# Optimization experiments

Measured on AMD Instinct MI355X. Metric: run time of the kernel, lower is better.

Reference implementation:

```python
import jax, jax.numpy as jnp
import numpy as np

ANNEALING_SCALE = 0.1
BS, NV, S, D, V = 2, 16, 1024, 768, 50257

def setup_inputs() -> dict:
    key = jax.random.key(0)
    k1, k2, k3, k4, k5 = jax.random.split(key, 5)
    return {
        "input_ids": jax.random.randint(k1, (BS, S), 0, V),
        "content": jax.random.normal(k2, (BS, NV, S, D), dtype=jnp.float32),
        "contextualization": jax.random.normal(k3, (BS, NV, S, S), dtype=jnp.float32) * 0.05,
        "lm_head_weight": jax.random.normal(k4, (V, D), dtype=jnp.float32) * 0.02,
        "content_weights": jax.random.uniform(k5, (V, NV), dtype=jnp.float32),
    }

def reference(input_ids, content, contextualization, lm_head_weight, content_weights):
    bs, nv, s, d = content.shape
    # --- mask_annealing ---
    # Original computes relu(content @ W.T) over full vocab then gathers at input_ids.
    # Equivalent: gather rows of W first, then contract (same math since relu is
    # elementwise and only gathered columns are summed).
    Wg = lm_head_weight[input_ids]                              # (bs, s, d)
    sims = jnp.einsum('bkid,bjd->bkij', content, Wg)            # (bs, 16, s, s)
    sims = jnp.sum(jax.nn.relu(sims), axis=3)                   # (bs, 16, s)
    scores = jax.nn.sigmoid(-ANNEALING_SCALE * sims + 6.0)
    # upweight_nearby modifier
    scores = scores * (1.0 + jnp.arange(s, dtype=content.dtype) / 100.0)[None, None, :]
    scores = jnp.transpose(scores, (0, 2, 1))                   # (bs, s, 16)
    # --- create_content_soft_mask ---
    cw = content_weights[input_ids]                             # (bs, s, 16)
    weights = cw * scores + (1.0 - scores)                      # (bs, s, 16)
    # --- weighted sense combination ---
    content_m = content * jnp.transpose(weights, (0, 2, 1))[..., None]  # (bs,16,s,d)
    hidden = jnp.einsum('bkij,bkjd->bid', contextualization, content_m) # (bs, s, d)
    logits = hidden @ lm_head_weight.T                          # (bs, s, vocab)
    return logits
```

## Files before the change

### kernel.cpp

```cpp
#include <hip/hip_runtime.h>
#include <cstdint>
#include <cstddef>

#define BSZ 2
#define NV 16
#define SEQ 1024
#define DIM 768
#define VOC 50257
#define VOCP 50304

typedef unsigned int u32;
typedef unsigned short u16;
typedef _Float16 half8 __attribute__((ext_vector_type(8)));
typedef float f32x4 __attribute__((ext_vector_type(4)));

__device__ __forceinline__ u16 f2h(float f) {
  return __builtin_bit_cast(unsigned short, (_Float16)f);
}
__device__ __forceinline__ u32 pk2h(float a, float b) {
  return (u32)f2h(a) | ((u32)f2h(b) << 16);
}

__device__ __forceinline__ void gload16(const u16* g, u16* l) {
  __builtin_amdgcn_global_load_lds(
      (const __attribute__((address_space(1))) void*)g,
      (__attribute__((address_space(3))) void*)l, 16, 0, 0);
}

__global__ void k_prep_content(const float* __restrict__ content,
                               u16* __restrict__ cbf, u16* __restrict__ cT) {
  __shared__ u16 tile[64][70];
  const int bk = blockIdx.z;
  const int d0 = blockIdx.x * 64, j0 = blockIdx.y * 64;
  const float* src = content + (size_t)bk * SEQ * DIM;
  u16* dst = cbf + (size_t)bk * SEQ * DIM;
  u16* dstT = cT + (size_t)bk * DIM * SEQ;
  const int c4 = (threadIdx.x & 15) * 4;
  const int r0 = threadIdx.x >> 4;
#pragma unroll
  for (int it = 0; it < 4; ++it) {
    const int r = it * 16 + r0;
    const float4 f = *(const float4*)(src + (size_t)(j0 + r) * DIM + d0 + c4);
    const u32 lo = pk2h(f.x, f.y), hi = pk2h(f.z, f.w);
    *(uint2*)(dst + (size_t)(j0 + r) * DIM + d0 + c4) = make_uint2(lo, hi);
    *(u32*)&tile[r][c4] = lo;
    *(u32*)&tile[r][c4 + 2] = hi;
  }
  __syncthreads();
#pragma unroll
  for (int it = 0; it < 4; ++it) {
    const int dd = it * 16 + r0;
    const int j4 = c4;
    const u32 lo = (u32)tile[j4][dd] | ((u32)tile[j4 + 1][dd] << 16);
    const u32 hi = (u32)tile[j4 + 2][dd] | ((u32)tile[j4 + 3][dd] << 16);
    *(uint2*)(dstT + (size_t)(d0 + dd) * SEQ + j0 + j4) = make_uint2(lo, hi);
  }
}

__global__ void k_prep_w(const float* __restrict__ W, u16* __restrict__ Wb) {
  const int v = blockIdx.x;
  const int c = threadIdx.x * 4;
  u32 lo, hi;
  if (v < VOC) {
    const float4 f = *(const float4*)(W + (size_t)v * DIM + c);
    lo = pk2h(f.x, f.y); hi = pk2h(f.z, f.w);
  } else {
    lo = 0u; hi = 0u;
  }
  *(uint2*)(Wb + (size_t)v * DIM + c) = make_uint2(lo, hi);
}

__global__ void k_gather(const int* __restrict__ ids, const u16* __restrict__ Wb,
                         u16* __restrict__ Wg) {
  const int b = blockIdx.y, j = blockIdx.x;
  const int row = ids[b * SEQ + j];
  const int c = threadIdx.x * 4;
  *(uint2*)(Wg + ((size_t)b * SEQ + j) * DIM + c) =
      *(const uint2*)(Wb + (size_t)row * DIM + c);
}

__global__ void k_zero(float* __restrict__ p, int n) {
  const int i = blockIdx.x * 256 + threadIdx.x;
  if (i < n) p[i] = 0.f;
}

template <int LDA, int LDB>
__device__ __forceinline__ void gemm_ring1(const u16* __restrict__ A,
                                           const u16* __restrict__ B,
                                           u16* As, u16* Bs,
                                           f32x4 (&acc)[4][4], int t) {
  const int lane = t & 63, w = t >> 6, wr = w >> 1, wc = w & 1;
  const int rl = lane & 15;
  const int gsw = (((lane >> 4) ^ ((rl >> 1) & 3)) * 8);
  const int srow = 16 * w + (lane >> 2);
  const int sg = (((lane & 3) ^ ((lane >> 3) & 3)) * 8);
  const size_t gaBase = (size_t)srow * LDA + sg;
  const size_t gbBase = (size_t)srow * LDB + sg;
  const int wof = w * 512;

#define STG1_(ss, kt)                                                   \
  {                                                                     \
    const u16* ga_ = A + gaBase + (size_t)(kt) * 32;                    \
    const u16* gb_ = B + gbBase + (size_t)(kt) * 32;                    \
    gload16(ga_, As + (ss) * 4096 + wof);                               \
    gload16(ga_ + (size_t)64 * LDA, As + (ss) * 4096 + wof + 2048);     \
    gload16(gb_, Bs + (ss) * 4096 + wof);                               \
    gload16(gb_ + (size_t)64 * LDB, Bs + (ss) * 4096 + wof + 2048);     \
  }

  STG1_(0, 0);
  STG1_(1, 1);
#pragma unroll 1
  for (int kt = 0; kt < 32; ++kt) {
    if (kt < 31)
      asm volatile("s_waitcnt vmcnt(4)" ::: "memory");
    else
      asm volatile("s_waitcnt vmcnt(0)" ::: "memory");
    __builtin_amdgcn_s_barrier();
    __builtin_amdgcn_sched_barrier(0);
    const int ss = kt % 3;
    if (kt < 30) STG1_((kt + 2) % 3, kt + 2);
    half8 af[4], bf[4];
#pragma unroll
    for (int m = 0; m < 4; ++m)
      af[m] = *(const half8*)(As + ss * 4096 + (wr * 64 + m * 16 + rl) * 32 + gsw);
#pragma unroll
    for (int n = 0; n < 4; ++n)
      bf[n] = *(const half8*)(Bs + ss * 4096 + (wc * 64 + n * 16 + rl) * 32 + gsw);
    __builtin_amdgcn_s_setprio(1);
#pragma unroll
    for (int m = 0; m < 4; ++m)
#pragma unroll
      for (int n = 0; n < 4; ++n)
        acc[m][n] = __builtin_amdgcn_mfma_f32_16x16x32_f16(af[m], bf[n], acc[m][n], 0, 0, 0);
    __builtin_amdgcn_s_setprio(0);
  }
#undef STG1_
}

template <int LDA, int LDB>
__device__ __forceinline__ void gemm_ring2(const u16* __restrict__ A0,
                                           const u16* __restrict__ A1,
                                           const u16* __restrict__ B, int ksteps,
                                           u16* As0, u16* As1, u16* Bs,
                                           f32x4 (&acc0)[4][4],
                                           f32x4 (&acc1)[4][4], int t) {
  const int lane = t & 63, w = t >> 6, wr = w >> 1, wc = w & 1;
  const int rl = lane & 15;
  const int gsw = (((lane >> 4) ^ ((rl >> 1) & 3)) * 8);
  const int srow = 16 * w + (lane >> 2);
  const int sg = (((lane & 3) ^ ((lane >> 3) & 3)) * 8);
  const size_t gaBase = (size_t)srow * LDA + sg;
  const size_t gbBase = (size_t)srow * LDB + sg;
  const int wof = w * 512;

#define STG3_(ss, kt)                                                   \
  {                                                                     \
    const u16* ga0_ = A0 + gaBase + (size_t)(kt) * 32;                  \
    const u16* ga1_ = A1 + gaBase + (size_t)(kt) * 32;                  \
    const u16* gb_ = B + gbBase + (size_t)(kt) * 32;                    \
    gload16(ga0_, As0 + (ss) * 4096 + wof);                             \
    gload16(ga0_ + (size_t)64 * LDA, As0 + (ss) * 4096 + wof + 2048);   \
    gload16(ga1_, As1 + (ss) * 4096 + wof);                            \
    gload16(ga1_ + (size_t)64 * LDA, As1 + (ss) * 4096 + wof + 2048);   \
    gload16(gb_, Bs + (ss) * 4096 + wof);                              \
    gload16(gb_ + (size_t)64 * LDB, Bs + (ss) * 4096 + wof + 2048);     \
  }

#define FRAGS3_(ss)                                                     \
  half8 af0[4], af1[4], bf[4];                                          \
  _Pragma("unroll") for (int n = 0; n < 4; ++n)                         \
      bf[n] = *(const half8*)(Bs + (ss) * 4096 +                        \
                              (wc * 64 + n * 16 + rl) * 32 + gsw);      \
  _Pragma("unroll") for (int m = 0; m < 4; ++m)                         \
      af0[m] = *(const half8*)(As0 + (ss) * 4096 +                      \
                               (wr * 64 + m * 16 + rl) * 32 + gsw);     \
  _Pragma("unroll") for (int m = 0; m < 4; ++m)                         \
      af1[m] = *(const half8*)(As1 + (ss) * 4096 +                      \
                               (wr * 64 + m * 16 + rl) * 32 + gsw);

#define MFMA32_                                                         \
  __builtin_amdgcn_s_setprio(1);                                        \
  _Pragma("unroll") for (int m = 0; m < 4; ++m)                         \
      _Pragma("unroll") for (int n = 0; n < 4; ++n)                     \
          acc0[m][n] = __builtin_amdgcn_mfma_f32_16x16x32_f16(          \
              af0[m], bf[n], acc0[m][n], 0, 0, 0);                      \
  _Pragma("unroll") for (int m = 0; m < 4; ++m)                         \
      _Pragma("unroll") for (int n = 0; n < 4; ++n)                     \
          acc1[m][n] = __builtin_amdgcn_mfma_f32_16x16x32_f16(          \
              af1[m], bf[n], acc1[m][n], 0, 0, 0);                      \
  __builtin_amdgcn_s_setprio(0);

#define STEPF_(ss, kt)                                                  \
  asm volatile("s_waitcnt vmcnt(6)" ::: "memory");                      \
  __builtin_amdgcn_s_barrier();                                         \
  __builtin_amdgcn_sched_barrier(0);                                    \
  STG3_(((ss) + 2) % 3, (kt) + 2);                                      \
  { FRAGS3_(ss) MFMA32_ }

#define STEPL6_(ss)                                                     \
  asm volatile("s_waitcnt vmcnt(6)" ::: "memory");                      \
  __builtin_amdgcn_s_barrier();                                         \
  __builtin_amdgcn_sched_barrier(0);                                    \
  { FRAGS3_(ss) MFMA32_ }

#define STEPL0_(ss)                                                     \
  asm volatile("s_waitcnt vmcnt(0)" ::: "memory");                      \
  __builtin_amdgcn_s_barrier();                                         \
  __builtin_amdgcn_sched_barrier(0);                                    \
  { FRAGS3_(ss) MFMA32_ }

  STG3_(0, 0);
  STG3_(1, 1);
  const int nTrip = ksteps / 3;
  for (int u = 0; u < nTrip - 1; ++u) {
    const int kt = 3 * u;
    STEPF_(0, kt);
    STEPF_(1, kt + 1);
    STEPF_(2, kt + 2);
  }
  STEPF_(0, ksteps - 3);
  STEPL6_(1);
  STEPL0_(2);
#undef STG3_
#undef FRAGS3_
#undef MFMA32_
#undef STEPF_
#undef STEPL6_
#undef STEPL0_
}

__global__ __launch_bounds__(256, 2) void k_sims(const u16* __restrict__ cbf,
                                                 const u16* __restrict__ Wg,
                                                 float* __restrict__ sims) {
  __shared__ __align__(16) u16 As0[3 * 4096];
  __shared__ __align__(16) u16 As1[3 * 4096];
  __shared__ __align__(16) u16 Bs[3 * 4096];
  const int bk = blockIdx.z, b = bk >> 4;
  const int t = threadIdx.x;
  const int i0 = blockIdx.y * 256;
  const u16* A0 = cbf + (size_t)bk * SEQ * DIM + (size_t)i0 * DIM;
  const u16* A1 = A0 + (size_t)128 * DIM;
  const u16* B = Wg + (size_t)b * SEQ * DIM + (size_t)(blockIdx.x * 128) * DIM;
  f32x4 acc0[4][4] = {}, acc1[4][4] = {};
  gemm_ring2<DIM, DIM>(A0, A1, B, DIM / 32, As0, As1, Bs, acc0, acc1, t);
  const int lane = t & 63, w = t >> 6, wr = w >> 1;
  const int rg = lane >> 4, cl = lane & 15;
#pragma unroll
  for (int m = 0; m < 4; ++m) {
#pragma unroll
    for (int r = 0; r < 4; ++r) {
      float s0 = 0.f, s1 = 0.f;
#pragma unroll
      for (int n = 0; n < 4; ++n) {
        s0 += fmaxf(acc0[m][n][r], 0.f);
        s1 += fmaxf(acc1[m][n][r], 0.f);
      }
      s0 += __shfl_xor(s0, 1); s1 += __shfl_xor(s1, 1);
      s0 += __shfl_xor(s0, 2); s1 += __shfl_xor(s1, 2);
      s0 += __shfl_xor(s0, 4); s1 += __shfl_xor(s1, 4);
      s0 += __shfl_xor(s0, 8); s1 += __shfl_xor(s1, 8);
      if (cl == 0) {
        const int i = i0 + wr * 64 + m * 16 + rg * 4 + r;
        atomicAdd(&sims[(size_t)bk * SEQ + i], s0);
        atomicAdd(&sims[(size_t)bk * SEQ + i + 128], s1);
      }
    }
  }
}

__global__ void k_weights(const float* __restrict__ sims, const int* __restrict__ ids,
                          const float* __restrict__ cw, float* __restrict__ wtsT) {
  const int j = blockIdx.x * 256 + threadIdx.x;
  const int bk = blockIdx.y;
  const int b = bk >> 4, k = bk & 15;
  const float sm = sims[(size_t)bk * SEQ + j];
  float score = 1.f / (1.f + __expf(0.1f * sm - 6.f));
  score *= 1.f + (float)j * 0.01f;
  const int id = ids[b * SEQ + j];
  const float c = cw[(size_t)id * NV + k];
  wtsT[(size_t)bk * SEQ + j] = c * score + (1.f - score);
}

__global__ void k_ctx(const float* __restrict__ ctx, const float* __restrict__ wtsT,
                      u16* __restrict__ ctxw) {
  const size_t i = ((size_t)blockIdx.x * 256 + threadIdx.x) * 4;
  const float4 c = *(const float4*)(ctx + i);
  const size_t bk = i >> 20;
  const int j = (int)(i & (SEQ - 1));
  const float4 wv = *(const float4*)(wtsT + bk * SEQ + j);
  *(uint2*)(ctxw + i) =
      make_uint2(pk2h(c.x * wv.x, c.y * wv.y), pk2h(c.z * wv.z, c.w * wv.w));
}

__global__ __launch_bounds__(256, 3) void k_hidden(const u16* __restrict__ ctxw,
                                                   const u16* __restrict__ cT,
                                                   float* __restrict__ part) {
  __shared__ __align__(16) u16 As[3 * 4096];
  __shared__ __align__(16) u16 Bs[3 * 4096];
  const int z = blockIdx.z;
  const int b = z >> 3, g = z & 7;
  const int i0 = blockIdx.y * 128, d0 = blockIdx.x * 128;
  const int t = threadIdx.x;
  f32x4 acc[4][4] = {};
  for (int kk = 0; kk < 2; ++kk) {
    const int sense = g * 2 + kk;
    const u16* A = ctxw + ((size_t)(b * NV + sense) * SEQ + i0) * SEQ;
    const u16* B = cT + ((size_t)(b * NV + sense) * DIM + d0) * SEQ;
    gemm_ring1<SEQ, SEQ>(A, B, As, Bs, acc, t);
    __syncthreads();
  }
  const int lane = t & 63, w = t >> 6, wr = w >> 1, wc = w & 1;
  const int rg = lane >> 4, cl = lane & 15;
  float* P = part + ((size_t)(g * BSZ + b) * SEQ + i0) * DIM + d0;
#pragma unroll
  for (int m = 0; m < 4; ++m)
#pragma unroll
    for (int n = 0; n < 4; ++n)
#pragma unroll
      for (int r = 0; r < 4; ++r)
        P[(size_t)(wr * 64 + m * 16 + rg * 4 + r) * DIM + wc * 64 + n * 16 + cl] =
            acc[m][n][r];
}

__global__ void k_reduce(const float* __restrict__ part, u16* __restrict__ hid) {
  const size_t i = ((size_t)blockIdx.x * 256 + threadIdx.x) * 4;
  const size_t NHID = (size_t)BSZ * SEQ * DIM;
  float4 s = {0.f, 0.f, 0.f, 0.f};
#pragma unroll
  for (int g = 0; g < 8; ++g) {
    const float4 p = *(const float4*)(part + (size_t)g * NHID + i);
    s.x += p.x; s.y += p.y; s.z += p.z; s.w += p.w;
  }
  *(uint2*)(hid + i) = make_uint2(pk2h(s.x, s.y), pk2h(s.z, s.w));
}

__global__ __launch_bounds__(256, 2) void k_logits(const u16* __restrict__ hid,
                                                   const u16* __restrict__ Wb,
                                                   float* __restrict__ out) {
  __shared__ __align__(16) u16 lds[3 * 12288];
  const int bid = blockIdx.x;
  const int swz = (bid & 7) * 393 + (bid >> 3);
  const int it = swz & 7, vt = swz >> 3;
  const int i0 = it * 256, v0 = vt * 128;
  const int t = threadIdx.x;
  const int lane = t & 63, w = t >> 6;
  const int wm = w >> 1, wn = w & 1;
  const int rl = lane & 15, kg = lane >> 4;
  const int gsw = (kg ^ ((rl >> 1) & 3)) * 8;
  const int srow = t >> 2;
  const int sgr = ((t & 3) ^ ((srow >> 1) & 3)) * 8;
  const u16* Abase = hid + ((size_t)i0 + srow) * DIM + sgr;
  const u16* Bbase = Wb + ((size_t)v0 + srow) * DIM + sgr;
  u16* dls = lds + t * 8;

#define STG(ss, koff)                                                 \
  {                                                                   \
    const u16* a_ = Abase + (koff);                                   \
    u16* d_ = dls + (ss) * 12288;                                     \
    gload16(a_, d_);                                                  \
    gload16(a_ + (size_t)64 * DIM, d_ + 2048);                        \
    gload16(a_ + (size_t)128 * DIM, d_ + 4096);                       \
    gload16(a_ + (size_t)192 * DIM, d_ + 6144);                       \
    const u16* b_ = Bbase + (koff);                                   \
    gload16(b_, d_ + 8192);                                           \
    gload16(b_ + (size_t)64 * DIM, d_ + 10240);                       \
  }

#define CMP(ss)                                                       \
  {                                                                   \
    half8 af[8], bf[4];                                               \
    _Pragma("unroll") for (int n = 0; n < 4; ++n)                     \
        bf[n] = *(const half8*)(lds + (ss) * 12288 + 8192 +           \
                                (wn * 64 + n * 16 + rl) * 32 + gsw);  \
    _Pragma("unroll") for (int m = 0; m < 8; ++m)                     \
        af[m] = *(const half8*)(lds + (ss) * 12288 +                  \
                                (wm * 128 + m * 16 + rl) * 32 + gsw); \
    __builtin_amdgcn_s_setprio(1);                                    \
    _Pragma("unroll") for (int m = 0; m < 8; ++m)                     \
        _Pragma("unroll") for (int n = 0; n < 4; ++n)                 \
            acc[m][n] = __builtin_amdgcn_mfma_f32_16x16x32_f16(       \
                af[m], bf[n], acc[m][n], 0, 0, 0);                    \
    __builtin_amdgcn_s_setprio(0);                                    \
  }

#define BARS                                                          \
  __builtin_amdgcn_s_barrier();                                       \
  __builtin_amdgcn_sched_barrier(0);

#define STEPF(ss, st, koff)                                           \
  asm volatile("s_waitcnt vmcnt(6)" ::: "memory");                    \
  BARS;                                                               \
  STG(st, koff);                                                      \
  CMP(ss)

  f32x4 acc[8][4] = {};
  STG(0, 0);
  STG(1, 32);
#pragma unroll 1
  for (int u = 0; u < 7; ++u) {
    const int kb = u * 96;
    STEPF(0, 2, kb + 64);
    STEPF(1, 0, kb + 96);
    STEPF(2, 1, kb + 128);
  }
  STEPF(0, 2, 736);
  asm volatile("s_waitcnt vmcnt(6)" ::: "memory");
  BARS;
  CMP(1);
  asm volatile("s_waitcnt vmcnt(0)" ::: "memory");
  BARS;
  CMP(2);
#undef STG
#undef CMP
#undef BARS
#undef STEPF

#pragma unroll
  for (int m = 0; m < 8; ++m)
#pragma unroll
    for (int n = 0; n < 4; ++n) {
      const int vv = v0 + wn * 64 + n * 16 + rl;
      if (vv < VOC) {
        const int ib = i0 + wm * 128 + m * 16 + kg * 4;
#pragma unroll
        for (int r = 0; r < 4; ++r)
          out[(size_t)(ib + r) * VOC + vv] = acc[m][n][r];
      }
    }
}

extern "C" void kernel_launch(void* const* d_in, const int* in_sizes, int n_in,
                              void* d_out, int out_size, void* d_ws, size_t ws_size,
                              hipStream_t stream) {
  const int* ids = (const int*)d_in[0];
  const float* content = (const float*)d_in[1];
  const float* ctx = (const float*)d_in[2];
  const float* W = (const float*)d_in[3];
  const float* cw = (const float*)d_in[4];
  float* out = (float*)d_out;
  char* ws = (char*)d_ws;

  u16* cbf  = (u16*)(ws);
  u16* cT   = (u16*)(ws + 50331648);
  u16* Wb   = (u16*)(ws + 100663296);
  u16* Wg   = (u16*)(ws + 177930240);
  u16* ctxw = (u16*)(ws + 181075968);
  float* sims = (float*)(ws + 248184832);
  float* wtsT = (float*)(ws + 248315904);
  float* part = (float*)cbf;
  u16* hid = Wg;

  k_prep_content<<<dim3(DIM / 64, SEQ / 64, BSZ * NV), 256, 0, stream>>>(
      content, cbf, cT);
  k_prep_w<<<VOCP, 192, 0, stream>>>(W, Wb);
  k_gather<<<dim3(SEQ, BSZ), 192, 0, stream>>>(ids, Wb, Wg);
  k_zero<<<128, 256, 0, stream>>>(sims, BSZ * NV * SEQ);
  k_sims<<<dim3(8, 4, BSZ * NV), 256, 0, stream>>>(cbf, Wg, sims);
  k_weights<<<dim3(4, BSZ * NV), 256, 0, stream>>>(sims, ids, cw, wtsT);
  k_ctx<<<32768, 256, 0, stream>>>(ctx, wtsT, ctxw);
  k_hidden<<<dim3(6, 8, 16), 256, 0, stream>>>(ctxw, cT, part);
  k_reduce<<<1536, 256, 0, stream>>>(part, hid);
  k_logits<<<8 * 393, 256, 0, stream>>>(hid, Wb, out);
}
```

Measured before the change: 564.1 us.

## Give each wave private LDS tiles to drop block barriers in logits GEMM

The logits GEMM now has each wave stage its own 128x32 A slice and 64x32 B slice into a private region of LDS with a 3-deep ring. Block-wide s_barrier calls are gone and waves sync only through vmcnt/lgkmcnt waits. This removes barrier stalls between waves but duplicates A/B loads across waves, raises LDS use to 144KB, and drops occupancy to one block per CU. Separately, the weight fp16 conversion kernel becomes a grid-stride flat loop with 2048 blocks instead of one block per vocabulary row.

```diff
diff --git a/kernel.cpp b/kernel.cpp
--- a/kernel.cpp
+++ b/kernel.cpp
@@ -58,16 +58,17 @@
 }
 
 __global__ void k_prep_w(const float* __restrict__ W, u16* __restrict__ Wb) {
-  const int v = blockIdx.x;
-  const int c = threadIdx.x * 4;
-  u32 lo, hi;
-  if (v < VOC) {
-    const float4 f = *(const float4*)(W + (size_t)v * DIM + c);
-    lo = pk2h(f.x, f.y); hi = pk2h(f.z, f.w);
-  } else {
-    lo = 0u; hi = 0u;
-  }
-  *(uint2*)(Wb + (size_t)v * DIM + c) = make_uint2(lo, hi);
+  const size_t nW = (size_t)VOC * DIM / 4;
+  const size_t total = (size_t)VOCP * DIM / 4;
+  for (size_t u = (size_t)blockIdx.x * 256 + threadIdx.x; u < total;
+       u += (size_t)gridDim.x * 256) {
+    u32 lo = 0u, hi = 0u;
+    if (u < nW) {
+      const float4 f = *(const float4*)(W + u * 4);
+      lo = pk2h(f.x, f.y); hi = pk2h(f.z, f.w);
+    }
+    *(uint2*)(Wb + u * 4) = make_uint2(lo, hi);
+  }
 }
 
 __global__ void k_gather(const int* __restrict__ ids, const u16* __restrict__ Wb,
@@ -335,10 +336,10 @@
   *(uint2*)(hid + i) = make_uint2(pk2h(s.x, s.y), pk2h(s.z, s.w));
 }
 
-__global__ __launch_bounds__(256, 2) void k_logits(const u16* __restrict__ hid,
+__global__ __launch_bounds__(256, 1) void k_logits(const u16* __restrict__ hid,
                                                    const u16* __restrict__ Wb,
                                                    float* __restrict__ out) {
-  __shared__ __align__(16) u16 lds[3 * 12288];
+  __shared__ __align__(16) u16 lds[4 * 3 * 6144];
   const int bid = blockIdx.x;
   const int swz = (bid & 7) * 393 + (bid >> 3);
   const int it = swz & 7, vt = swz >> 3;
@@ -348,73 +349,64 @@
   const int wm = w >> 1, wn = w & 1;
   const int rl = lane & 15, kg = lane >> 4;
   const int gsw = (kg ^ ((rl >> 1) & 3)) * 8;
-  const int srow = t >> 2;
-  const int sgr = ((t & 3) ^ ((srow >> 1) & 3)) * 8;
-  const u16* Abase = hid + ((size_t)i0 + srow) * DIM + sgr;
-  const u16* Bbase = Wb + ((size_t)v0 + srow) * DIM + sgr;
-  u16* dls = lds + t * 8;
-
-#define STG(ss, koff)                                                 \
-  {                                                                   \
-    const u16* a_ = Abase + (koff);                                   \
-    u16* d_ = dls + (ss) * 12288;                                     \
-    gload16(a_, d_);                                                  \
-    gload16(a_ + (size_t)64 * DIM, d_ + 2048);                        \
-    gload16(a_ + (size_t)128 * DIM, d_ + 4096);                       \
-    gload16(a_ + (size_t)192 * DIM, d_ + 6144);                       \
-    const u16* b_ = Bbase + (koff);                                   \
-    gload16(b_, d_ + 8192);                                           \
-    gload16(b_ + (size_t)64 * DIM, d_ + 10240);                       \
-  }
-
-#define CMP(ss)                                                       \
-  {                                                                   \
-    half8 af[8], bf[4];                                               \
-    _Pragma("unroll") for (int n = 0; n < 4; ++n)                     \
-        bf[n] = *(const half8*)(lds + (ss) * 12288 + 8192 +           \
-                                (wn * 64 + n * 16 + rl) * 32 + gsw);  \
-    _Pragma("unroll") for (int m = 0; m < 8; ++m)                     \
-        af[m] = *(const half8*)(lds + (ss) * 12288 +                  \
-                                (wm * 128 + m * 16 + rl) * 32 + gsw); \
-    __builtin_amdgcn_s_setprio(1);                                    \
-    _Pragma("unroll") for (int m = 0; m < 8; ++m)                     \
-        _Pragma("unroll") for (int n = 0; n < 4; ++n)                 \
-            acc[m][n] = __builtin_amdgcn_mfma_f32_16x16x32_f16(       \
-                af[m], bf[n], acc[m][n], 0, 0, 0);                    \
-    __builtin_amdgcn_s_setprio(0);                                    \
-  }
-
-#define BARS                                                          \
-  __builtin_amdgcn_s_barrier();                                       \
-  __builtin_amdgcn_sched_barrier(0);
-
-#define STEPF(ss, st, koff)                                           \
-  asm volatile("s_waitcnt vmcnt(6)" ::: "memory");                    \
-  BARS;                                                               \
-  STG(st, koff);                                                      \
-  CMP(ss)
+  const int sgr = ((lane & 3) ^ ((lane >> 3) & 3)) * 8;
+  const u16* Aw = hid + ((size_t)i0 + wm * 128 + (lane >> 2)) * DIM + sgr;
+  const u16* Bw = Wb + ((size_t)v0 + wn * 64 + (lane >> 2)) * DIM + sgr;
+  u16* wbase = lds + w * 18432;
+  u16* dls = wbase + lane * 8;
+
+#define STG(ss, koff)                                                  \
+  {                                                                    \
+    const u16* a_ = Aw + (koff);                                       \
+    u16* d_ = dls + (ss) * 6144;                                       \
+    gload16(a_, d_);                                                   \
+    gload16(a_ + (size_t)16 * DIM, d_ + 512);                          \
+    gload16(a_ + (size_t)32 * DIM, d_ + 1024);                         \
+    gload16(a_ + (size_t)48 * DIM, d_ + 1536);                         \
+    gload16(a_ + (size_t)64 * DIM, d_ + 2048);                         \
+    gload16(a_ + (size_t)80 * DIM, d_ + 2560);                         \
+    gload16(a_ + (size_t)96 * DIM, d_ + 3072);                         \
+    gload16(a_ + (size_t)112 * DIM, d_ + 3584);                        \
+    const u16* b_ = Bw + (koff);                                       \
+    u16* e_ = d_ + 4096;                                               \
+    gload16(b_, e_);                                                   \
+    gload16(b_ + (size_t)16 * DIM, e_ + 512);                          \
+    gload16(b_ + (size_t)32 * DIM, e_ + 1024);                         \
+    gload16(b_ + (size_t)48 * DIM, e_ + 1536);                         \
+  }
 
   f32x4 acc[8][4] = {};
   STG(0, 0);
   STG(1, 32);
 #pragma unroll 1
-  for (int u = 0; u < 7; ++u) {
-    const int kb = u * 96;
-    STEPF(0, 2, kb + 64);
-    STEPF(1, 0, kb + 96);
-    STEPF(2, 1, kb + 128);
-  }
-  STEPF(0, 2, 736);
-  asm volatile("s_waitcnt vmcnt(6)" ::: "memory");
-  BARS;
-  CMP(1);
-  asm volatile("s_waitcnt vmcnt(0)" ::: "memory");
-  BARS;
-  CMP(2);
+  for (int k = 0; k < 24; ++k) {
+    if (k < 23)
+      asm volatile("s_waitcnt vmcnt(12)" ::: "memory");
+    else
+      asm volatile("s_waitcnt vmcnt(0)" ::: "memory");
+    __builtin_amdgcn_sched_barrier(0);
+    const int ss = k % 3;
+    const u16* sa = wbase + ss * 6144;
+    half8 af[8], bf[4];
+#pragma unroll
+    for (int n = 0; n < 4; ++n)
+      bf[n] = *(const half8*)(sa + 4096 + (n * 16 + rl) * 32 + gsw);
+#pragma unroll
+    for (int m = 0; m < 8; ++m)
+      af[m] = *(const half8*)(sa + (m * 16 + rl) * 32 + gsw);
+    if (k < 22) STG((k + 2) % 3, (k + 2) * 32);
+    asm volatile("s_waitcnt lgkmcnt(0)" ::: "memory");
+    __builtin_amdgcn_sched_barrier(0);
+    __builtin_amdgcn_s_setprio(1);
+#pragma unroll
+    for (int m = 0; m < 8; ++m)
+#pragma unroll
+      for (int n = 0; n < 4; ++n)
+        acc[m][n] =
+            __builtin_amdgcn_mfma_f32_16x16x32_f16(af[m], bf[n], acc[m][n], 0, 0, 0);
+    __builtin_amdgcn_s_setprio(0);
+  }
 #undef STG
-#undef CMP
-#undef BARS
-#undef STEPF
 
 #pragma unroll
   for (int m = 0; m < 8; ++m)
@@ -453,7 +445,7 @@
 
   k_prep_content<<<dim3(DIM / 64, SEQ / 64, BSZ * NV), 256, 0, stream>>>(
       content, cbf, cT);
-  k_prep_w<<<VOCP, 192, 0, stream>>>(W, Wb);
+  k_prep_w<<<2048, 256, 0, stream>>>(W, Wb);
   k_gather<<<dim3(SEQ, BSZ), 192, 0, stream>>>(ids, Wb, Wg);
   k_zero<<<128, 256, 0, stream>>>(sims, BSZ * NV * SEQ);
   k_sims<<<dim3(8, 4, BSZ * NV), 256, 0, stream>>>(cbf, Wg, sims);
```

Result: slower. 651.0 us (+15.4%).

## Fuse context weighting into hidden GEMM with register-staged loads

Applied to the files above, without the earlier changes.

Removes the separate k_ctx pass that wrote a weighted fp16 copy of the 128MB contextualization tensor. k_hidden now reads the fp32 context and sense weights directly, multiplies and converts them in registers, then stores the result to a double-buffered LDS tile. This replaces the async global-to-LDS triple-buffer ring with a register prefetch and two barriers per k-step. Blocks are remapped to a 1D grid so that co-resident blocks share content tiles. k_prep_w also becomes a grid-stride kernel. The fused loop reads fp32 (twice the bytes of fp16) and has less prefetch depth, which could leave the MFMA units waiting on memory.

```diff
diff --git a/kernel.cpp b/kernel.cpp
--- a/kernel.cpp
+++ b/kernel.cpp
@@ -58,16 +58,17 @@
 }
 
 __global__ void k_prep_w(const float* __restrict__ W, u16* __restrict__ Wb) {
-  const int v = blockIdx.x;
-  const int c = threadIdx.x * 4;
-  u32 lo, hi;
-  if (v < VOC) {
-    const float4 f = *(const float4*)(W + (size_t)v * DIM + c);
-    lo = pk2h(f.x, f.y); hi = pk2h(f.z, f.w);
-  } else {
-    lo = 0u; hi = 0u;
-  }
-  *(uint2*)(Wb + (size_t)v * DIM + c) = make_uint2(lo, hi);
+  const size_t nW = (size_t)VOC * DIM / 4;
+  const size_t total = (size_t)VOCP * DIM / 4;
+  for (size_t u = (size_t)blockIdx.x * 256 + threadIdx.x; u < total;
+       u += (size_t)gridDim.x * 256) {
+    u32 lo = 0u, hi = 0u;
+    if (u < nW) {
+      const float4 f = *(const float4*)(W + u * 4);
+      lo = pk2h(f.x, f.y); hi = pk2h(f.z, f.w);
+    }
+    *(uint2*)(Wb + u * 4) = make_uint2(lo, hi);
+  }
 }
 
 __global__ void k_gather(const int* __restrict__ ids, const u16* __restrict__ Wb,
@@ -82,60 +83,6 @@
 __global__ void k_zero(float* __restrict__ p, int n) {
   const int i = blockIdx.x * 256 + threadIdx.x;
   if (i < n) p[i] = 0.f;
-}
-
-template <int LDA, int LDB>
-__device__ __forceinline__ void gemm_ring1(const u16* __restrict__ A,
-                                           const u16* __restrict__ B,
-                                           u16* As, u16* Bs,
-                                           f32x4 (&acc)[4][4], int t) {
-  const int lane = t & 63, w = t >> 6, wr = w >> 1, wc = w & 1;
-  const int rl = lane & 15;
-  const int gsw = (((lane >> 4) ^ ((rl >> 1) & 3)) * 8);
-  const int srow = 16 * w + (lane >> 2);
-  const int sg = (((lane & 3) ^ ((lane >> 3) & 3)) * 8);
-  const size_t gaBase = (size_t)srow * LDA + sg;
-  const size_t gbBase = (size_t)srow * LDB + sg;
-  const int wof = w * 512;
-
-#define STG1_(ss, kt)                                                   \
-  {                                                                     \
-    const u16* ga_ = A + gaBase + (size_t)(kt) * 32;                    \
-    const u16* gb_ = B + gbBase + (size_t)(kt) * 32;                    \
-    gload16(ga_, As + (ss) * 4096 + wof);                               \
-    gload16(ga_ + (size_t)64 * LDA, As + (ss) * 4096 + wof + 2048);     \
-    gload16(gb_, Bs + (ss) * 4096 + wof);                               \
-    gload16(gb_ + (size_t)64 * LDB, Bs + (ss) * 4096 + wof + 2048);     \
-  }
-
-  STG1_(0, 0);
-  STG1_(1, 1);
-#pragma unroll 1
-  for (int kt = 0; kt < 32; ++kt) {
-    if (kt < 31)
-      asm volatile("s_waitcnt vmcnt(4)" ::: "memory");
-    else
-      asm volatile("s_waitcnt vmcnt(0)" ::: "memory");
-    __builtin_amdgcn_s_barrier();
-    __builtin_amdgcn_sched_barrier(0);
-    const int ss = kt % 3;
-    if (kt < 30) STG1_((kt + 2) % 3, kt + 2);
-    half8 af[4], bf[4];
-#pragma unroll
-    for (int m = 0; m < 4; ++m)
-      af[m] = *(const half8*)(As + ss * 4096 + (wr * 64 + m * 16 + rl) * 32 + gsw);
-#pragma unroll
-    for (int n = 0; n < 4; ++n)
-      bf[n] = *(const half8*)(Bs + ss * 4096 + (wc * 64 + n * 16 + rl) * 32 + gsw);
-    __builtin_amdgcn_s_setprio(1);
-#pragma unroll
-    for (int m = 0; m < 4; ++m)
-#pragma unroll
-      for (int n = 0; n < 4; ++n)
-        acc[m][n] = __builtin_amdgcn_mfma_f32_16x16x32_f16(af[m], bf[n], acc[m][n], 0, 0, 0);
-    __builtin_amdgcn_s_setprio(0);
-  }
-#undef STG1_
 }
 
 template <int LDA, int LDB>
@@ -282,37 +229,95 @@
   wtsT[(size_t)bk * SEQ + j] = c * score + (1.f - score);
 }
 
-__global__ void k_ctx(const float* __restrict__ ctx, const float* __restrict__ wtsT,
-                      u16* __restrict__ ctxw) {
-  const size_t i = ((size_t)blockIdx.x * 256 + threadIdx.x) * 4;
-  const float4 c = *(const float4*)(ctx + i);
-  const size_t bk = i >> 20;
-  const int j = (int)(i & (SEQ - 1));
-  const float4 wv = *(const float4*)(wtsT + bk * SEQ + j);
-  *(uint2*)(ctxw + i) =
-      make_uint2(pk2h(c.x * wv.x, c.y * wv.y), pk2h(c.z * wv.z, c.w * wv.w));
-}
-
-__global__ __launch_bounds__(256, 3) void k_hidden(const u16* __restrict__ ctxw,
+__global__ __launch_bounds__(256, 3) void k_hidden(const float* __restrict__ ctx,
+                                                   const float* __restrict__ wtsT,
                                                    const u16* __restrict__ cT,
                                                    float* __restrict__ part) {
-  __shared__ __align__(16) u16 As[3 * 4096];
-  __shared__ __align__(16) u16 Bs[3 * 4096];
-  const int z = blockIdx.z;
-  const int b = z >> 3, g = z & 7;
-  const int i0 = blockIdx.y * 128, d0 = blockIdx.x * 128;
+  __shared__ __align__(16) u16 As[2 * 4096];
+  __shared__ __align__(16) u16 Bs[2 * 4096];
+  const int L = blockIdx.x;
+  const int g8 = L & 7, q = L >> 3;
+  const int p = g8 * 16 + q / 6;
+  const int dt = q % 6;
+  const int y = p & 7, z = p >> 3;
+  const int b = z >> 3, grp = z & 7;
+  const int i0 = y * 128, d0 = dt * 128;
   const int t = threadIdx.x;
+  const int lane = t & 63, w = t >> 6, wr = w >> 1, wc = w & 1;
+  const int rl = lane & 15;
+  const int gsw = (((lane >> 4) ^ ((rl >> 1) & 3)) * 8);
+  const int srow = 16 * w + (lane >> 2);
+  const int sg = (((lane & 3) ^ ((lane >> 3) & 3)) * 8);
+
   f32x4 acc[4][4] = {};
-  for (int kk = 0; kk < 2; ++kk) {
-    const int sense = g * 2 + kk;
-    const u16* A = ctxw + ((size_t)(b * NV + sense) * SEQ + i0) * SEQ;
-    const u16* B = cT + ((size_t)(b * NV + sense) * DIM + d0) * SEQ;
-    gemm_ring1<SEQ, SEQ>(A, B, As, Bs, acc, t);
+  float4 ra0, ra1, ra2, ra3, rw0, rw1;
+  uint4 rb0, rb1;
+
+#define LDREGS(u_)                                                      \
+  {                                                                     \
+    const int s_ = (u_) >> 5, kt_ = (u_) & 31;                          \
+    const size_t bkq_ = (size_t)b * NV + grp * 2 + s_;                  \
+    const int jsw_ = kt_ * 32 + sg;                                     \
+    const float* ap_ = ctx + (bkq_ * SEQ + i0 + srow) * SEQ + jsw_;     \
+    ra0 = *(const float4*)(ap_);                                        \
+    ra1 = *(const float4*)(ap_ + 4);                                    \
+    ra2 = *(const float4*)(ap_ + (size_t)64 * SEQ);                     \
+    ra3 = *(const float4*)(ap_ + (size_t)64 * SEQ + 4);                 \
+    const float* wp_ = wtsT + bkq_ * SEQ + jsw_;                        \
+    rw0 = *(const float4*)(wp_);                                        \
+    rw1 = *(const float4*)(wp_ + 4);                                    \
+    const u16* bp_ = cT + (bkq_ * DIM + d0 + srow) * SEQ + jsw_;        \
+    rb0 = *(const uint4*)(bp_);                                         \
+    rb1 = *(const uint4*)(bp_ + (size_t)64 * SEQ);                      \
+  }
+
+#define WRITE(cc)                                                       \
+  {                                                                     \
+    u16* da_ = As + (cc) * 4096 + w * 512 + lane * 8;                   \
+    *(uint4*)(da_) =                                                    \
+        make_uint4(pk2h(ra0.x * rw0.x, ra0.y * rw0.y),                  \
+                   pk2h(ra0.z * rw0.z, ra0.w * rw0.w),                  \
+                   pk2h(ra1.x * rw1.x, ra1.y * rw1.y),                  \
+                   pk2h(ra1.z * rw1.z, ra1.w * rw1.w));                 \
+    *(uint4*)(da_ + 2048) =                                             \
+        make_uint4(pk2h(ra2.x * rw0.x, ra2.y * rw0.y),                  \
+                   pk2h(ra2.z * rw0.z, ra2.w * rw0.w),                  \
+                   pk2h(ra3.x * rw1.x, ra3.y * rw1.y),                  \
+                   pk2h(ra3.z * rw1.z, ra3.w * rw1.w));                 \
+    u16* db_ = Bs + (cc) * 4096 + w * 512 + lane * 8;                   \
+    *(uint4*)(db_) = rb0;                                               \
+    *(uint4*)(db_ + 2048) = rb1;                                        \
+  }
+
+  LDREGS(0);
+  int cur = 0;
+#pragma unroll 1
+  for (int u = 0; u < 64; ++u) {
     __syncthreads();
-  }
-  const int lane = t & 63, w = t >> 6, wr = w >> 1, wc = w & 1;
+    WRITE(cur);
+    if (u < 63) LDREGS(u + 1);
+    __syncthreads();
+    half8 af[4], bf[4];
+#pragma unroll
+    for (int m = 0; m < 4; ++m)
+      af[m] = *(const half8*)(As + cur * 4096 + (wr * 64 + m * 16 + rl) * 32 + gsw);
+#pragma unroll
+    for (int n = 0; n < 4; ++n)
+      bf[n] = *(const half8*)(Bs + cur * 4096 + (wc * 64 + n * 16 + rl) * 32 + gsw);
+    __builtin_amdgcn_s_setprio(1);
+#pragma unroll
+    for (int m = 0; m < 4; ++m)
+#pragma unroll
+      for (int n = 0; n < 4; ++n)
+        acc[m][n] = __builtin_amdgcn_mfma_f32_16x16x32_f16(af[m], bf[n], acc[m][n], 0, 0, 0);
+    __builtin_amdgcn_s_setprio(0);
+    cur ^= 1;
+  }
+#undef LDREGS
+#undef WRITE
+
   const int rg = lane >> 4, cl = lane & 15;
-  float* P = part + ((size_t)(g * BSZ + b) * SEQ + i0) * DIM + d0;
+  float* P = part + ((size_t)(grp * BSZ + b) * SEQ + i0) * DIM + d0;
 #pragma unroll
   for (int m = 0; m < 4; ++m)
 #pragma unroll
@@ -445,7 +450,6 @@
   u16* cT   = (u16*)(ws + 50331648);
   u16* Wb   = (u16*)(ws + 100663296);
   u16* Wg   = (u16*)(ws + 177930240);
-  u16* ctxw = (u16*)(ws + 181075968);
   float* sims = (float*)(ws + 248184832);
   float* wtsT = (float*)(ws + 248315904);
   float* part = (float*)cbf;
@@ -453,13 +457,12 @@
 
   k_prep_content<<<dim3(DIM / 64, SEQ / 64, BSZ * NV), 256, 0, stream>>>(
       content, cbf, cT);
-  k_prep_w<<<VOCP, 192, 0, stream>>>(W, Wb);
+  k_prep_w<<<2048, 256, 0, stream>>>(W, Wb);
   k_gather<<<dim3(SEQ, BSZ), 192, 0, stream>>>(ids, Wb, Wg);
   k_zero<<<128, 256, 0, stream>>>(sims, BSZ * NV * SEQ);
   k_sims<<<dim3(8, 4, BSZ * NV), 256, 0, stream>>>(cbf, Wg, sims);
   k_weights<<<dim3(4, BSZ * NV), 256, 0, stream>>>(sims, ids, cw, wtsT);
-  k_ctx<<<32768, 256, 0, stream>>>(ctx, wtsT, ctxw);
-  k_hidden<<<dim3(6, 8, 16), 256, 0, stream>>>(ctxw, cT, part);
+  k_hidden<<<768, 256, 0, stream>>>(ctx, wtsT, cT, part);
   k_reduce<<<1536, 256, 0, stream>>>(part, hid);
   k_logits<<<8 * 393, 256, 0, stream>>>(hid, Wb, out);
 }
```

After: 549.7 us, median of 3. 1.03x faster.
